# Optimization experiments

Hardware: AMD Instinct MI355X
Metric: run time of the kernel (lower is better)

## Reference

```python
import jax, jax.numpy as jnp
import numpy as np

NEG_SLOPE = 0.2  # PyG GATConv default negative_slope


def _glorot(key, shape):
    fan = shape[0]
    return jax.random.normal(key, shape, dtype=jnp.float32) / np.sqrt(fan)


def setup_inputs() -> dict:
    key = jax.random.key(0)
    ks = jax.random.split(key, 32)
    N, E, C_IN, C_H, C_OUT = 20000, 320000, 128, 640, 2
    inp = {
        "x": jax.random.normal(ks[0], (N, C_IN), dtype=jnp.float32),
        "edge_index": jax.random.randint(ks[1], (2, E), 0, N, dtype=jnp.int64),
    }
    dims = [(C_IN, C_H), (C_H, C_H), (C_H, C_H), (C_H, C_H), (C_H, C_OUT)]
    for i, (ci, co) in enumerate(dims, start=1):
        k = jax.random.split(ks[1 + i], 4)
        inp[f"W{i}"] = _glorot(k[0], (ci, co))
        inp[f"as{i}"] = _glorot(k[1], (co,))
        inp[f"ad{i}"] = _glorot(k[2], (co,))
        inp[f"b{i}"] = jnp.zeros((co,), dtype=jnp.float32)
    return inp


def _gat_conv(h, W, a_src, a_dst, b, src, dst, N):
    # h: [N, Ci] -> hW: [N, Co]
    hW = h @ W
    # per-edge attention logit: LeakyReLU(alpha_src[j] + alpha_dst[i]) for edge j->i
    e = jax.nn.leaky_relu((hW @ a_src)[src] + (hW @ a_dst)[dst], NEG_SLOPE)
    # segment softmax over incoming edges of each dst node (self-loops guarantee nonempty)
    m = jax.ops.segment_max(e, dst, num_segments=N)
    ex = jnp.exp(e - m[dst])
    den = jax.ops.segment_sum(ex, dst, num_segments=N)
    alpha = ex / den[dst]
    # weighted scatter-add of source messages
    out = jax.ops.segment_sum(alpha[:, None] * hW[src], dst, num_segments=N)
    return out + b


def reference(x, edge_index, W1, as1, ad1, b1, W2, as2, ad2, b2, W3, as3, ad3, b3,
              W4, as4, ad4, b4, W5, as5, ad5, b5):
    N = x.shape[0]
    # PyG GATConv default add_self_loops=True
    loops = jnp.arange(N, dtype=edge_index.dtype)
    ei = jnp.concatenate([edge_index, jnp.stack([loops, loops])], axis=1)
    src, dst = ei[0], ei[1]
    h = jax.nn.relu(_gat_conv(x, W1, as1, ad1, b1, src, dst, N))
    h = jax.nn.relu(_gat_conv(h, W2, as2, ad2, b2, src, dst, N))
    h = jax.nn.relu(_gat_conv(h, W3, as3, ad3, b3, src, dst, N))
    h = jax.nn.relu(_gat_conv(h, W4, as4, ad4, b4, src, dst, N))
    # dropout in eval mode = identity
    return _gat_conv(h, W5, as5, ad5, b5, src, dst, N)
```

## Files before the change

kernel.cpp:

```cpp
#include <hip/hip_runtime.h>
#include <math.h>

#define N_NODES 20000
#define MPAD 20096
#define E_EDGES 320000
#define ET (E_EDGES + N_NODES)
#define C_HID 640
#define C_IN 128
#define NEG_SLOPE 0.2f

typedef __attribute__((ext_vector_type(8))) short bf16x8;
typedef __attribute__((ext_vector_type(4))) float f32x4;

__device__ __forceinline__ float leaky(float x) { return x > 0.f ? x : NEG_SLOPE * x; }

__device__ __forceinline__ unsigned short f2bf(float f) {
    unsigned u = __float_as_uint(f);
    unsigned r = (u + 0x7fffu + ((u >> 16) & 1u)) >> 16;
    return (unsigned short)r;
}
__device__ __forceinline__ float bf2f(unsigned short h) {
    return __uint_as_float(((unsigned)h) << 16);
}

__device__ __forceinline__ void gld16(const void* g, void* l) {
    __builtin_amdgcn_global_load_lds((const __attribute__((address_space(1))) unsigned int*)g,
                                     (__attribute__((address_space(3))) unsigned int*)l,
                                     16, 0, 0);
}

__global__ void k_zero(int* p, int n) {
    int i = blockIdx.x * blockDim.x + threadIdx.x;
    if (i < n) p[i] = 0;
}

__global__ void k_zerof(float* p, int n) {
    int i = blockIdx.x * blockDim.x + threadIdx.x;
    if (i < n) p[i] = 0.f;
}

__global__ void k_count(const int* __restrict__ ei, int* __restrict__ counts) {
    int j = blockIdx.x * blockDim.x + threadIdx.x;
    if (j >= ET) return;
    int d = (j < E_EDGES) ? ei[E_EDGES + j] : (j - E_EDGES);
    atomicAdd(&counts[d], 1);
}

__global__ __launch_bounds__(1024) void k_scan(int* __restrict__ counts,
                                               int* __restrict__ rowptr) {
    __shared__ int part[1024];
    int t = threadIdx.x;
    int base = t * 20;
    int incl[20];
    int s = 0;
#pragma unroll
    for (int k = 0; k < 20; k++) {
        int i = base + k;
        int v = (i < N_NODES) ? counts[i] : 0;
        s += v;
        incl[k] = s;
    }
    part[t] = s;
    __syncthreads();
    for (int off = 1; off < 1024; off <<= 1) {
        int x = (t >= off) ? part[t - off] : 0;
        __syncthreads();
        part[t] += x;
        __syncthreads();
    }
    int prefix = (t == 0) ? 0 : part[t - 1];
    if (t == 0) rowptr[0] = 0;
#pragma unroll
    for (int k = 0; k < 20; k++) {
        int i = base + k;
        if (i < N_NODES) {
            rowptr[i + 1] = prefix + incl[k];
            counts[i] = (k == 0) ? prefix : prefix + incl[k - 1];
        }
    }
}

__global__ void k_fill(const int* __restrict__ ei, int* __restrict__ cursor, int* __restrict__ col) {
    int j = blockIdx.x * blockDim.x + threadIdx.x;
    if (j >= ET) return;
    int s, d;
    if (j < E_EDGES) { s = ei[j]; d = ei[E_EDGES + j]; }
    else { s = d = j - E_EDGES; }
    int pos = atomicAdd(&cursor[d], 1);
    col[pos] = s;
}

__global__ void k_splitW(const float* __restrict__ W, unsigned short* __restrict__ Wth,
                         unsigned short* __restrict__ Wtl, int K) {
    int idx = blockIdx.x * blockDim.x + threadIdx.x;
    if (idx >= K * C_HID) return;
    int k = idx / C_HID, n = idx - k * C_HID;
    float w = W[idx];
    unsigned short h = f2bf(w);
    Wth[n * K + k] = h;
    Wtl[n * K + k] = f2bf(w - bf2f(h));
}

__global__ void k_padzero(unsigned short* __restrict__ xah, unsigned short* __restrict__ xal,
                          unsigned short* __restrict__ ph, unsigned short* __restrict__ pl) {
    int idx = blockIdx.x * blockDim.x + threadIdx.x;
    const int nx = (MPAD - N_NODES) * C_IN;
    const int np = (MPAD - N_NODES) * C_HID;
    if (idx < nx) {
        xah[N_NODES * C_IN + idx] = 0;
        xal[N_NODES * C_IN + idx] = 0;
    }
    if (idx < np) {
        ph[N_NODES * C_HID + idx] = 0;
        pl[N_NODES * C_HID + idx] = 0;
    }
}

__global__ void k_wa(const float* __restrict__ W, const float* __restrict__ a_s,
                     const float* __restrict__ a_d,
                     float* __restrict__ ws_, float* __restrict__ wd_) {
    int wave = (blockIdx.x * blockDim.x + threadIdx.x) >> 6;
    int lane = threadIdx.x & 63;
    if (wave >= C_IN) return;
    const float* row = W + (size_t)wave * C_HID;
    float s = 0.f, d = 0.f;
#pragma unroll
    for (int c = lane; c < C_HID; c += 64) {
        float w = row[c];
        s = fmaf(w, a_s[c], s);
        d = fmaf(w, a_d[c], d);
    }
    for (int o = 32; o; o >>= 1) { s += __shfl_xor(s, o); d += __shfl_xor(d, o); }
    if (lane == 0) { ws_[wave] = s; wd_[wave] = d; }
}

__global__ __launch_bounds__(256) void k_logitx(const float* __restrict__ x,
                                                const float* __restrict__ ws_,
                                                const float* __restrict__ wd_,
                                                float* __restrict__ as_, float* __restrict__ ad_) {
    int wave = (blockIdx.x * blockDim.x + threadIdx.x) >> 6;
    int lane = threadIdx.x & 63;
    if (wave >= N_NODES) return;
    float2 xv = ((const float2*)(x + (size_t)wave * C_IN))[lane];
    float2 wsv = ((const float2*)ws_)[lane];
    float2 wdv = ((const float2*)wd_)[lane];
    float s = xv.x * wsv.x + xv.y * wsv.y;
    float d = xv.x * wdv.x + xv.y * wdv.y;
    for (int o = 32; o; o >>= 1) { s += __shfl_xor(s, o); d += __shfl_xor(d, o); }
    if (lane == 0) { as_[wave] = s; ad_[wave] = d; }
}

__global__ __launch_bounds__(256) void k_mfma_gemm(
    const unsigned short* __restrict__ Ahi, const unsigned short* __restrict__ Alo,
    const unsigned short* __restrict__ Bth, const unsigned short* __restrict__ Btl,
    float* __restrict__ C, int K, int M,
    const float* __restrict__ asrc, const float* __restrict__ adst,
    float* __restrict__ as_, float* __restrict__ ad_) {
    __shared__ unsigned short lds[4 * 128 * 32];
    const int t = threadIdx.x;
    const int lane = t & 63, wv = t >> 6;
    const int wm = wv & 1, wn = wv >> 1;
    const int quad = lane >> 4, cl = lane & 15;
    const int rowBase = blockIdx.x * 128;
    const int colBase = blockIdx.y * 128;
    const int r = t >> 2, c8 = (t & 3) * 8;

    f32x4 acc[4][4];
#pragma unroll
    for (int i = 0; i < 4; i++)
#pragma unroll
        for (int j = 0; j < 4; j++)
            acc[i][j] = (f32x4){0.f, 0.f, 0.f, 0.f};

    for (int k0 = 0; k0 < K; k0 += 32) {
        __syncthreads();
#pragma unroll
        for (int p = 0; p < 2; ++p) {
            int row = p * 64 + r;
            size_t ga = (size_t)(rowBase + row) * K + k0 + c8;
            size_t gb = (size_t)(colBase + row) * K + k0 + c8;
            int lo = row * 32 + c8;
            gld16(Ahi + ga, &lds[lo]);
            gld16(Alo + ga, &lds[4096 + lo]);
            gld16(Bth + gb, &lds[8192 + lo]);
            gld16(Btl + gb, &lds[12288 + lo]);
        }
        __syncthreads();

        bf16x8 ah[4], al[4], bh[4], bl[4];
#pragma unroll
        for (int i = 0; i < 4; ++i) {
            int am = (wm * 64 + i * 16 + cl) * 32 + quad * 8;
            ah[i] = *(const bf16x8*)&lds[am];
            al[i] = *(const bf16x8*)&lds[4096 + am];
            int bn = (wn * 64 + i * 16 + cl) * 32 + quad * 8;
            bh[i] = *(const bf16x8*)&lds[8192 + bn];
            bl[i] = *(const bf16x8*)&lds[12288 + bn];
        }
#pragma unroll
        for (int i = 0; i < 4; ++i)
#pragma unroll
            for (int j = 0; j < 4; ++j) {
                acc[i][j] = __builtin_amdgcn_mfma_f32_16x16x32_bf16(ah[i], bh[j], acc[i][j], 0, 0, 0);
                acc[i][j] = __builtin_amdgcn_mfma_f32_16x16x32_bf16(ah[i], bl[j], acc[i][j], 0, 0, 0);
                acc[i][j] = __builtin_amdgcn_mfma_f32_16x16x32_bf16(al[i], bh[j], acc[i][j], 0, 0, 0);
            }
    }

#pragma unroll
    for (int i = 0; i < 4; ++i)
#pragma unroll
        for (int j = 0; j < 4; ++j) {
            int colC = colBase + wn * 64 + j * 16 + cl;
#pragma unroll
            for (int rr = 0; rr < 4; ++rr) {
                int rowC = rowBase + wm * 64 + i * 16 + quad * 4 + rr;
                if (rowC < M) C[(size_t)rowC * C_HID + colC] = acc[i][j][rr];
            }
        }

    float av[4], dv[4];
#pragma unroll
    for (int j = 0; j < 4; ++j) {
        int cn = colBase + wn * 64 + j * 16 + cl;
        av[j] = asrc[cn];
        dv[j] = adst[cn];
    }
#pragma unroll
    for (int i = 0; i < 4; ++i)
#pragma unroll
        for (int rr = 0; rr < 4; ++rr) {
            float s = 0.f, d = 0.f;
#pragma unroll
            for (int j = 0; j < 4; ++j) {
                float v = acc[i][j][rr];
                s = fmaf(v, av[j], s);
                d = fmaf(v, dv[j], d);
            }
#pragma unroll
            for (int o = 8; o >= 1; o >>= 1) {
                s += __shfl_xor(s, o);
                d += __shfl_xor(d, o);
            }
            int rowC = rowBase + wm * 64 + i * 16 + quad * 4 + rr;
            if (cl == 0 && rowC < M) {
                atomicAdd(&as_[rowC], s);
                atomicAdd(&ad_[rowC], d);
            }
        }
}

__global__ __launch_bounds__(256) void k_mfma_gemm_pair(
    const unsigned short* __restrict__ Ahi, const unsigned short* __restrict__ Alo,
    const unsigned short* __restrict__ Bth, const unsigned short* __restrict__ Btl,
    unsigned short* __restrict__ Oh, unsigned short* __restrict__ Ol,
    const float* __restrict__ bias, int K, int M) {
    __shared__ unsigned short lds[4 * 128 * 32];
    const int t = threadIdx.x;
    const int lane = t & 63, wv = t >> 6;
    const int wm = wv & 1, wn = wv >> 1;
    const int quad = lane >> 4, cl = lane & 15;
    const int rowBase = blockIdx.x * 128;
    const int colBase = blockIdx.y * 128;
    const int r = t >> 2, c8 = (t & 3) * 8;

    f32x4 acc[4][4];
#pragma unroll
    for (int i = 0; i < 4; i++)
#pragma unroll
        for (int j = 0; j < 4; j++)
            acc[i][j] = (f32x4){0.f, 0.f, 0.f, 0.f};

    for (int k0 = 0; k0 < K; k0 += 32) {
        __syncthreads();
#pragma unroll
        for (int p = 0; p < 2; ++p) {
            int row = p * 64 + r;
            size_t ga = (size_t)(rowBase + row) * K + k0 + c8;
            size_t gb = (size_t)(colBase + row) * K + k0 + c8;
            int lo = row * 32 + c8;
            gld16(Ahi + ga, &lds[lo]);
            gld16(Alo + ga, &lds[4096 + lo]);
            gld16(Bth + gb, &lds[8192 + lo]);
            gld16(Btl + gb, &lds[12288 + lo]);
        }
        __syncthreads();

        bf16x8 ah[4], al[4], bh[4], bl[4];
#pragma unroll
        for (int i = 0; i < 4; ++i) {
            int am = (wm * 64 + i * 16 + cl) * 32 + quad * 8;
            ah[i] = *(const bf16x8*)&lds[am];
            al[i] = *(const bf16x8*)&lds[4096 + am];
            int bn = (wn * 64 + i * 16 + cl) * 32 + quad * 8;
            bh[i] = *(const bf16x8*)&lds[8192 + bn];
            bl[i] = *(const bf16x8*)&lds[12288 + bn];
        }
#pragma unroll
        for (int i = 0; i < 4; ++i)
#pragma unroll
            for (int j = 0; j < 4; ++j) {
                acc[i][j] = __builtin_amdgcn_mfma_f32_16x16x32_bf16(ah[i], bh[j], acc[i][j], 0, 0, 0);
                acc[i][j] = __builtin_amdgcn_mfma_f32_16x16x32_bf16(ah[i], bl[j], acc[i][j], 0, 0, 0);
                acc[i][j] = __builtin_amdgcn_mfma_f32_16x16x32_bf16(al[i], bh[j], acc[i][j], 0, 0, 0);
            }
    }

#pragma unroll
    for (int j = 0; j < 4; ++j) {
        int colC = colBase + wn * 64 + j * 16 + cl;
        float bv = bias[colC];
#pragma unroll
        for (int i = 0; i < 4; ++i)
#pragma unroll
            for (int rr = 0; rr < 4; ++rr) {
                int rowC = rowBase + wm * 64 + i * 16 + quad * 4 + rr;
                if (rowC < M) {
                    float v = fmaxf(acc[i][j][rr] + bv, 0.f);
                    unsigned short h = f2bf(v);
                    Oh[(size_t)rowC * C_HID + colC] = h;
                    Ol[(size_t)rowC * C_HID + colC] = f2bf(v - bf2f(h));
                }
            }
    }
}

__global__ __launch_bounds__(256) void k_gather(const float* __restrict__ hW,
                                                const float* __restrict__ as_,
                                                const float* __restrict__ ad_,
                                                const int* __restrict__ rowptr,
                                                const int* __restrict__ col,
                                                const float* __restrict__ bias,
                                                unsigned short* __restrict__ outh,
                                                unsigned short* __restrict__ outl) {
    int wv = threadIdx.x >> 6, lane = threadIdx.x & 63;
    int node = blockIdx.x * 4 + wv;
    int c = blockIdx.y;
    if (node >= N_NODES) return;
    int start = rowptr[node], end = rowptr[node + 1];
    int deg = end - start;
    const float* base = hW + c * 128 + lane * 2;
    float ax = 0.f, ay = 0.f;
    float adi = ad_[node];

    if (deg <= 64) {
        int col_v = col[start + min(lane, deg - 1)];
        float asv = as_[col_v];
        float logit = (lane < deg) ? leaky(asv + adi) : -1e30f;
        float m = logit;
#pragma unroll
        for (int o = 32; o; o >>= 1) m = fmaxf(m, __shfl_xor(m, o));
        float ex = __expf(logit - m);
        float den = ex;
#pragma unroll
        for (int o = 32; o; o >>= 1) den += __shfl_xor(den, o);
        float alpha_v = ex / den;

        for (int e0 = 0; e0 < deg; e0 += 8) {
            float2 r[8];
            float a[8];
#pragma unroll
            for (int q = 0; q < 8; ++q) {
                int e = e0 + q;
                int ec = min(e, deg - 1);
                int s = __shfl(col_v, ec);
                float ar = __shfl(alpha_v, ec);
                a[q] = (e < deg) ? ar : 0.f;
                r[q] = *(const float2*)(base + (size_t)s * C_HID);
            }
#pragma unroll
            for (int q = 0; q < 8; ++q) {
                ax = fmaf(a[q], r[q].x, ax);
                ay = fmaf(a[q], r[q].y, ay);
            }
        }
    } else {
        float m = -1e30f;
        for (int j = start + lane; j < end; j += 64)
            m = fmaxf(m, leaky(as_[col[j]] + adi));
        for (int o = 32; o; o >>= 1) m = fmaxf(m, __shfl_xor(m, o));
        float den = 0.f;
        for (int j = start + lane; j < end; j += 64)
            den += __expf(leaky(as_[col[j]] + adi) - m);
        for (int o = 32; o; o >>= 1) den += __shfl_xor(den, o);
        float inv = 1.f / den;
        for (int j = start; j < end; ++j) {
            int s = col[j];
            float a = __expf(leaky(as_[s] + adi) - m) * inv;
            float2 r = *(const float2*)(base + (size_t)s * C_HID);
            ax = fmaf(a, r.x, ax);
            ay = fmaf(a, r.y, ay);
        }
    }

    float2 b = *(const float2*)&bias[c * 128 + lane * 2];
    float v0 = fmaxf(ax + b.x, 0.f);
    float v1 = fmaxf(ay + b.y, 0.f);
    unsigned short h0 = f2bf(v0), h1 = f2bf(v1);
    size_t o = (size_t)node * C_HID + c * 128 + lane * 2;
    *(ushort2*)&outh[o] = make_ushort2(h0, h1);
    *(ushort2*)&outl[o] = make_ushort2(f2bf(v0 - bf2f(h0)), f2bf(v1 - bf2f(h1)));
}

__global__ __launch_bounds__(256) void k_gather_x(const float* __restrict__ x,
                                                  const float* __restrict__ as_,
                                                  const float* __restrict__ ad_,
                                                  const int* __restrict__ rowptr,
                                                  const int* __restrict__ col,
                                                  unsigned short* __restrict__ outh,
                                                  unsigned short* __restrict__ outl) {
    int wv = threadIdx.x >> 6, lane = threadIdx.x & 63;
    int node = blockIdx.x * 4 + wv;
    if (node >= N_NODES) return;
    int start = rowptr[node], end = rowptr[node + 1];
    int deg = end - start;
    const float* base = x + lane * 2;
    float ax = 0.f, ay = 0.f;
    float adi = ad_[node];

    if (deg <= 64) {
        int col_v = col[start + min(lane, deg - 1)];
        float asv = as_[col_v];
        float logit = (lane < deg) ? leaky(asv + adi) : -1e30f;
        float m = logit;
#pragma unroll
        for (int o = 32; o; o >>= 1) m = fmaxf(m, __shfl_xor(m, o));
        float ex = __expf(logit - m);
        float den = ex;
#pragma unroll
        for (int o = 32; o; o >>= 1) den += __shfl_xor(den, o);
        float alpha_v = ex / den;

        for (int e0 = 0; e0 < deg; e0 += 8) {
            float2 r[8];
            float a[8];
#pragma unroll
            for (int q = 0; q < 8; ++q) {
                int e = e0 + q;
                int ec = min(e, deg - 1);
                int s = __shfl(col_v, ec);
                float ar = __shfl(alpha_v, ec);
                a[q] = (e < deg) ? ar : 0.f;
                r[q] = *(const float2*)(base + (size_t)s * C_IN);
            }
#pragma unroll
            for (int q = 0; q < 8; ++q) {
                ax = fmaf(a[q], r[q].x, ax);
                ay = fmaf(a[q], r[q].y, ay);
            }
        }
    } else {
        float m = -1e30f;
        for (int j = start + lane; j < end; j += 64)
            m = fmaxf(m, leaky(as_[col[j]] + adi));
        for (int o = 32; o; o >>= 1) m = fmaxf(m, __shfl_xor(m, o));
        float den = 0.f;
        for (int j = start + lane; j < end; j += 64)
            den += __expf(leaky(as_[col[j]] + adi) - m);
        for (int o = 32; o; o >>= 1) den += __shfl_xor(den, o);
        float inv = 1.f / den;
        for (int j = start; j < end; ++j) {
            int s = col[j];
            float a = __expf(leaky(as_[s] + adi) - m) * inv;
            float2 r = *(const float2*)(base + (size_t)s * C_IN);
            ax = fmaf(a, r.x, ax);
            ay = fmaf(a, r.y, ay);
        }
    }

    unsigned short h0 = f2bf(ax), h1 = f2bf(ay);
    size_t o = (size_t)node * C_IN + lane * 2;
    *(ushort2*)&outh[o] = make_ushort2(h0, h1);
    *(ushort2*)&outl[o] = make_ushort2(f2bf(ax - bf2f(h0)), f2bf(ay - bf2f(h1)));
}

__global__ __launch_bounds__(256) void k_gemm2(const unsigned short* __restrict__ hh,
                                               const unsigned short* __restrict__ hl,
                                               const float* __restrict__ W,
                                               const float* __restrict__ asrc,
                                               const float* __restrict__ adst,
                                               float* __restrict__ hW5,
                                               float* __restrict__ as_,
                                               float* __restrict__ ad_) {
    int wave = (blockIdx.x * blockDim.x + threadIdx.x) >> 6;
    int lane = threadIdx.x & 63;
    if (wave >= N_NODES) return;
    const ushort2* rh = (const ushort2*)(hh + (size_t)wave * C_HID);
    const ushort2* rl = (const ushort2*)(hl + (size_t)wave * C_HID);
    float a0 = 0.f, a1 = 0.f;
#pragma unroll
    for (int k2 = lane; k2 < C_HID / 2; k2 += 64) {
        ushort2 h2 = rh[k2];
        ushort2 l2 = rl[k2];
        float v0 = bf2f(h2.x) + bf2f(l2.x);
        float v1 = bf2f(h2.y) + bf2f(l2.y);
        int k = k2 * 2;
        a0 = fmaf(v0, W[k * 2 + 0], a0);
        a1 = fmaf(v0, W[k * 2 + 1], a1);
        a0 = fmaf(v1, W[k * 2 + 2], a0);
        a1 = fmaf(v1, W[k * 2 + 3], a1);
    }
    for (int o = 32; o; o >>= 1) { a0 += __shfl_xor(a0, o); a1 += __shfl_xor(a1, o); }
    if (lane == 0) {
        hW5[wave * 2 + 0] = a0;
        hW5[wave * 2 + 1] = a1;
        as_[wave] = a0 * asrc[0] + a1 * asrc[1];
        ad_[wave] = a0 * adst[0] + a1 * adst[1];
    }
}

__global__ __launch_bounds__(256) void k_agg2(const float* __restrict__ hW5,
                                              const float* __restrict__ as_,
                                              const float* __restrict__ ad_,
                                              const int* __restrict__ rowptr,
                                              const int* __restrict__ col,
                                              const float* __restrict__ bias,
                                              float* __restrict__ out) {
    int wv = threadIdx.x >> 6, lane = threadIdx.x & 63;
    int node = blockIdx.x * 4 + wv;
    if (node >= N_NODES) return;
    int start = rowptr[node], end = rowptr[node + 1];
    int deg = end - start;
    float adi = ad_[node];
    float o0, o1;
    if (deg <= 64) {
        int cv = col[start + min(lane, deg - 1)];
        float logit = (lane < deg) ? leaky(as_[cv] + adi) : -1e30f;
        float m = logit;
#pragma unroll
        for (int o = 32; o; o >>= 1) m = fmaxf(m, __shfl_xor(m, o));
        float ex = __expf(logit - m);
        float den = ex;
#pragma unroll
        for (int o = 32; o; o >>= 1) den += __shfl_xor(den, o);
        float al = ex / den;
        float2 hv = make_float2(0.f, 0.f);
        if (lane < deg) hv = *(const float2*)&hW5[cv * 2];
        o0 = al * hv.x; o1 = al * hv.y;
#pragma unroll
        for (int o = 32; o; o >>= 1) { o0 += __shfl_xor(o0, o); o1 += __shfl_xor(o1, o); }
    } else {
        float m = -1e30f;
        for (int j = start + lane; j < end; j += 64)
            m = fmaxf(m, leaky(as_[col[j]] + adi));
        for (int o = 32; o; o >>= 1) m = fmaxf(m, __shfl_xor(m, o));
        float den = 0.f;
        for (int j = start + lane; j < end; j += 64)
            den += __expf(leaky(as_[col[j]] + adi) - m);
        for (int o = 32; o; o >>= 1) den += __shfl_xor(den, o);
        float inv = 1.f / den;
        o0 = 0.f; o1 = 0.f;
        for (int j = start + lane; j < end; j += 64) {
            int s = col[j];
            float al = __expf(leaky(as_[s] + adi) - m) * inv;
            o0 = fmaf(al, hW5[s * 2 + 0], o0);
            o1 = fmaf(al, hW5[s * 2 + 1], o1);
        }
        for (int o = 32; o; o >>= 1) { o0 += __shfl_xor(o0, o); o1 += __shfl_xor(o1, o); }
    }
    if (lane == 0) {
        out[node * 2 + 0] = o0 + bias[0];
        out[node * 2 + 1] = o1 + bias[1];
    }
}

extern "C" void kernel_launch(void* const* d_in, const int* in_sizes, int n_in,
                              void* d_out, int out_size, void* d_ws, size_t ws_size,
                              hipStream_t stream) {
    const float* x   = (const float*)d_in[0];
    const int*   ei  = (const int*)d_in[1];
    const float* W[5]  = {(const float*)d_in[2],  (const float*)d_in[6],
                          (const float*)d_in[10], (const float*)d_in[14],
                          (const float*)d_in[18]};
    const float* As[5] = {(const float*)d_in[3],  (const float*)d_in[7],
                          (const float*)d_in[11], (const float*)d_in[15],
                          (const float*)d_in[19]};
    const float* Ad[5] = {(const float*)d_in[4],  (const float*)d_in[8],
                          (const float*)d_in[12], (const float*)d_in[16],
                          (const float*)d_in[20]};
    const float* Bi[5] = {(const float*)d_in[5],  (const float*)d_in[9],
                          (const float*)d_in[13], (const float*)d_in[17],
                          (const float*)d_in[21]};
    float* out = (float*)d_out;

    char* w = (char*)d_ws;
    float* bufX = (float*)w;                 w += (size_t)N_NODES * C_HID * 4;
    unsigned short* xa_hi = (unsigned short*)bufX;
    unsigned short* xa_lo = xa_hi + (size_t)MPAD * C_IN;
    unsigned short* pair_hi = (unsigned short*)w; w += (size_t)MPAD * C_HID * 2;
    unsigned short* pair_lo = (unsigned short*)w; w += (size_t)MPAD * C_HID * 2;
    unsigned short* Wth = (unsigned short*)w;     w += (size_t)C_HID * C_HID * 2;
    unsigned short* Wtl = (unsigned short*)w;     w += (size_t)C_HID * C_HID * 2;
    float* as_  = (float*)w;  w += N_NODES * 4;
    float* ad_  = (float*)w;  w += N_NODES * 4;
    float* hW5  = (float*)w;  w += N_NODES * 2 * 4;
    float* ws_  = (float*)w;  w += C_IN * 4;
    float* wd_  = (float*)w;  w += C_IN * 4;
    int* rowptr = (int*)w;    w += (N_NODES + 1) * 4 + 12;
    int* counts = (int*)w;    w += N_NODES * 4;
    int* col    = (int*)w;    w += ET * 4;

    const int TB = 256;
    k_zero<<<(N_NODES + TB - 1) / TB, TB, 0, stream>>>(counts, N_NODES);
    k_count<<<(ET + TB - 1) / TB, TB, 0, stream>>>(ei, counts);
    k_scan<<<1, 1024, 0, stream>>>(counts, rowptr);
    k_fill<<<(ET + TB - 1) / TB, TB, 0, stream>>>(ei, counts, col);

    k_padzero<<<((MPAD - N_NODES) * C_HID + TB - 1) / TB, TB, 0, stream>>>(xa_hi, xa_lo, pair_hi, pair_lo);

    dim3 gemmGrid(MPAD / 128, C_HID / 128);
    dim3 gathGrid(N_NODES / 4, 5);
    int nodeWaveBlocks = (N_NODES + 3) / 4;

    k_splitW<<<(C_IN * C_HID + TB - 1) / TB, TB, 0, stream>>>(W[0], Wth, Wtl, C_IN);
    k_wa<<<32, TB, 0, stream>>>(W[0], As[0], Ad[0], ws_, wd_);
    k_logitx<<<nodeWaveBlocks, TB, 0, stream>>>(x, ws_, wd_, as_, ad_);
    k_gather_x<<<nodeWaveBlocks, TB, 0, stream>>>(x, as_, ad_, rowptr, col, xa_hi, xa_lo);
    k_mfma_gemm_pair<<<gemmGrid, TB, 0, stream>>>(xa_hi, xa_lo, Wth, Wtl,
                                                  pair_hi, pair_lo, Bi[0], C_IN, N_NODES);

    for (int l = 1; l <= 3; ++l) {
        k_zerof<<<(2 * N_NODES + TB - 1) / TB, TB, 0, stream>>>(as_, 2 * N_NODES);
        k_splitW<<<(C_HID * C_HID + TB - 1) / TB, TB, 0, stream>>>(W[l], Wth, Wtl, C_HID);
        k_mfma_gemm<<<gemmGrid, TB, 0, stream>>>(pair_hi, pair_lo, Wth, Wtl, bufX, C_HID, N_NODES,
                                                 As[l], Ad[l], as_, ad_);
        k_gather<<<gathGrid, TB, 0, stream>>>(bufX, as_, ad_, rowptr, col, Bi[l], pair_hi, pair_lo);
    }

    k_gemm2<<<nodeWaveBlocks, TB, 0, stream>>>(pair_hi, pair_lo, W[4], As[4], Ad[4], hW5, as_, ad_);
    k_agg2<<<nodeWaveBlocks, TB, 0, stream>>>(hW5, as_, ad_, rowptr, col, Bi[4], out);
}
```

Measured before the change: 814.9 us.

## Use 128x64 GEMM tiles with swizzled block order and tiled weight transpose

The MFMA GEMM kernels shrink from 128x128 to 128x64 output tiles, using a 1D grid with a grouped block-index decode so neighbouring blocks share A row tiles. This doubles the block count to 1570 so more CUs stay busy, at the cost of reloading A tiles twice as often. The weight split/transpose kernel is rewritten to stage through a padded shared-memory tile, giving coalesced float4 reads and vectorized ushort4 writes in place of strided scalar stores.

```diff
diff --git a/kernel.cpp b/kernel.cpp
--- a/kernel.cpp
+++ b/kernel.cpp
@@ -9,6 +9,11 @@
 #define C_IN 128
 #define NEG_SLOPE 0.2f
 
+#define NXB 157
+#define NYB 10
+#define NXB_FULL 152
+#define IDS_MAIN 1520
+
 typedef __attribute__((ext_vector_type(8))) short bf16x8;
 typedef __attribute__((ext_vector_type(4))) float f32x4;
 
@@ -27,6 +32,18 @@
     __builtin_amdgcn_global_load_lds((const __attribute__((address_space(1))) unsigned int*)g,
                                      (__attribute__((address_space(3))) unsigned int*)l,
                                      16, 0, 0);
+}
+
+__device__ __forceinline__ void decode_xy(int id, int& bx, int& by) {
+    if (id < IDS_MAIN) {
+        int g = id / 80;
+        bx = g * 8 + (id & 7);
+        by = (id % 80) >> 3;
+    } else {
+        int v = id - IDS_MAIN;
+        bx = NXB_FULL + v % 5;
+        by = v / 5;
+    }
 }
 
 __global__ void k_zero(int* p, int n) {
@@ -90,15 +107,37 @@
     col[pos] = s;
 }
 
-__global__ void k_splitW(const float* __restrict__ W, unsigned short* __restrict__ Wth,
-                         unsigned short* __restrict__ Wtl, int K) {
-    int idx = blockIdx.x * blockDim.x + threadIdx.x;
-    if (idx >= K * C_HID) return;
-    int k = idx / C_HID, n = idx - k * C_HID;
-    float w = W[idx];
-    unsigned short h = f2bf(w);
-    Wth[n * K + k] = h;
-    Wtl[n * K + k] = f2bf(w - bf2f(h));
+__global__ __launch_bounds__(256) void k_splitWT(const float* __restrict__ W,
+                                                 unsigned short* __restrict__ Wth,
+                                                 unsigned short* __restrict__ Wtl, int K) {
+    __shared__ float tile[64][65];
+    int t = threadIdx.x;
+    int ki = blockIdx.x * 64, ni = blockIdx.y * 64;
+    int tr = t >> 2;
+    int tc = (t & 3) * 16;
+#pragma unroll
+    for (int q = 0; q < 4; ++q) {
+        float4 v = *(const float4*)&W[(size_t)(ki + tr) * C_HID + ni + tc + q * 4];
+        tile[tr][tc + q * 4 + 0] = v.x;
+        tile[tr][tc + q * 4 + 1] = v.y;
+        tile[tr][tc + q * 4 + 2] = v.z;
+        tile[tr][tc + q * 4 + 3] = v.w;
+    }
+    __syncthreads();
+    unsigned short hh[16], ll[16];
+#pragma unroll
+    for (int j = 0; j < 16; ++j) {
+        float w = tile[tc + j][tr];
+        unsigned short h = f2bf(w);
+        hh[j] = h;
+        ll[j] = f2bf(w - bf2f(h));
+    }
+    size_t o = (size_t)(ni + tr) * K + ki + tc;
+#pragma unroll
+    for (int q = 0; q < 4; ++q) {
+        *(ushort4*)&Wth[o + q * 4] = make_ushort4(hh[q*4], hh[q*4+1], hh[q*4+2], hh[q*4+3]);
+        *(ushort4*)&Wtl[o + q * 4] = make_ushort4(ll[q*4], ll[q*4+1], ll[q*4+2], ll[q*4+3]);
+    }
 }
 
 __global__ void k_padzero(unsigned short* __restrict__ xah, unsigned short* __restrict__ xal,
@@ -156,51 +195,59 @@
     float* __restrict__ C, int K, int M,
     const float* __restrict__ asrc, const float* __restrict__ adst,
     float* __restrict__ as_, float* __restrict__ ad_) {
-    __shared__ unsigned short lds[4 * 128 * 32];
+    __shared__ unsigned short lds[12288];
     const int t = threadIdx.x;
     const int lane = t & 63, wv = t >> 6;
-    const int wm = wv & 1, wn = wv >> 1;
+    const int wm = wv >> 1, wn = wv & 1;
     const int quad = lane >> 4, cl = lane & 15;
-    const int rowBase = blockIdx.x * 128;
-    const int colBase = blockIdx.y * 128;
-    const int r = t >> 2, c8 = (t & 3) * 8;
-
-    f32x4 acc[4][4];
+    int bx, by;
+    decode_xy(blockIdx.x, bx, by);
+    const int rowBase = bx * 128;
+    const int colBase = by * 64;
+    const int r4 = t >> 2, c8 = (t & 3) * 8;
+
+    f32x4 acc[4][2];
 #pragma unroll
     for (int i = 0; i < 4; i++)
 #pragma unroll
-        for (int j = 0; j < 4; j++)
+        for (int j = 0; j < 2; j++)
             acc[i][j] = (f32x4){0.f, 0.f, 0.f, 0.f};
 
     for (int k0 = 0; k0 < K; k0 += 32) {
         __syncthreads();
 #pragma unroll
         for (int p = 0; p < 2; ++p) {
-            int row = p * 64 + r;
+            int row = p * 64 + r4;
             size_t ga = (size_t)(rowBase + row) * K + k0 + c8;
-            size_t gb = (size_t)(colBase + row) * K + k0 + c8;
             int lo = row * 32 + c8;
             gld16(Ahi + ga, &lds[lo]);
             gld16(Alo + ga, &lds[4096 + lo]);
+        }
+        {
+            size_t gb = (size_t)(colBase + r4) * K + k0 + c8;
+            int lo = r4 * 32 + c8;
             gld16(Bth + gb, &lds[8192 + lo]);
-            gld16(Btl + gb, &lds[12288 + lo]);
+            gld16(Btl + gb, &lds[10240 + lo]);
         }
         __syncthreads();
 
-        bf16x8 ah[4], al[4], bh[4], bl[4];
+        bf16x8 ah[4], al[4], bh[2], bl[2];
 #pragma unroll
         for (int i = 0; i < 4; ++i) {
             int am = (wm * 64 + i * 16 + cl) * 32 + quad * 8;
             ah[i] = *(const bf16x8*)&lds[am];
             al[i] = *(const bf16x8*)&lds[4096 + am];
-            int bn = (wn * 64 + i * 16 + cl) * 32 + quad * 8;
-            bh[i] = *(const bf16x8*)&lds[8192 + bn];
-            bl[i] = *(const bf16x8*)&lds[12288 + bn];
+        }
+#pragma unroll
+        for (int j = 0; j < 2; ++j) {
+            int bn = (wn * 32 + j * 16 + cl) * 32 + quad * 8;
+            bh[j] = *(const bf16x8*)&lds[8192 + bn];
+            bl[j] = *(const bf16x8*)&lds[10240 + bn];
         }
 #pragma unroll
         for (int i = 0; i < 4; ++i)
 #pragma unroll
-            for (int j = 0; j < 4; ++j) {
+            for (int j = 0; j < 2; ++j) {
                 acc[i][j] = __builtin_amdgcn_mfma_f32_16x16x32_bf16(ah[i], bh[j], acc[i][j], 0, 0, 0);
                 acc[i][j] = __builtin_amdgcn_mfma_f32_16x16x32_bf16(ah[i], bl[j], acc[i][j], 0, 0, 0);
                 acc[i][j] = __builtin_amdgcn_mfma_f32_16x16x32_bf16(al[i], bh[j], acc[i][j], 0, 0, 0);
@@ -210,8 +257,8 @@
 #pragma unroll
     for (int i = 0; i < 4; ++i)
 #pragma unroll
-        for (int j = 0; j < 4; ++j) {
-            int colC = colBase + wn * 64 + j * 16 + cl;
+        for (int j = 0; j < 2; ++j) {
+            int colC = colBase + wn * 32 + j * 16 + cl;
 #pragma unroll
             for (int rr = 0; rr < 4; ++rr) {
                 int rowC = rowBase + wm * 64 + i * 16 + quad * 4 + rr;
@@ -219,10 +266,10 @@
             }
         }
 
-    float av[4], dv[4];
-#pragma unroll
-    for (int j = 0; j < 4; ++j) {
-        int cn = colBase + wn * 64 + j * 16 + cl;
+    float av[2], dv[2];
+#pragma unroll
+    for (int j = 0; j < 2; ++j) {
+        int cn = colBase + wn * 32 + j * 16 + cl;
         av[j] = asrc[cn];
         dv[j] = adst[cn];
     }
@@ -232,7 +279,7 @@
         for (int rr = 0; rr < 4; ++rr) {
             float s = 0.f, d = 0.f;
 #pragma unroll
-            for (int j = 0; j < 4; ++j) {
+            for (int j = 0; j < 2; ++j) {
                 float v = acc[i][j][rr];
                 s = fmaf(v, av[j], s);
                 d = fmaf(v, dv[j], d);
@@ -255,51 +302,59 @@
     const unsigned short* __restrict__ Bth, const unsigned short* __restrict__ Btl,
     unsigned short* __restrict__ Oh, unsigned short* __restrict__ Ol,
     const float* __restrict__ bias, int K, int M) {
-    __shared__ unsigned short lds[4 * 128 * 32];
+    __shared__ unsigned short lds[12288];
     const int t = threadIdx.x;
     const int lane = t & 63, wv = t >> 6;
-    const int wm = wv & 1, wn = wv >> 1;
+    const int wm = wv >> 1, wn = wv & 1;
     const int quad = lane >> 4, cl = lane & 15;
-    const int rowBase = blockIdx.x * 128;
-    const int colBase = blockIdx.y * 128;
-    const int r = t >> 2, c8 = (t & 3) * 8;
-
-    f32x4 acc[4][4];
+    int bx, by;
+    decode_xy(blockIdx.x, bx, by);
+    const int rowBase = bx * 128;
+    const int colBase = by * 64;
+    const int r4 = t >> 2, c8 = (t & 3) * 8;
+
+    f32x4 acc[4][2];
 #pragma unroll
     for (int i = 0; i < 4; i++)
 #pragma unroll
-        for (int j = 0; j < 4; j++)
+        for (int j = 0; j < 2; j++)
             acc[i][j] = (f32x4){0.f, 0.f, 0.f, 0.f};
 
     for (int k0 = 0; k0 < K; k0 += 32) {
         __syncthreads();
 #pragma unroll
         for (int p = 0; p < 2; ++p) {
-            int row = p * 64 + r;
+            int row = p * 64 + r4;
             size_t ga = (size_t)(rowBase + row) * K + k0 + c8;
-            size_t gb = (size_t)(colBase + row) * K + k0 + c8;
             int lo = row * 32 + c8;
             gld16(Ahi + ga, &lds[lo]);
             gld16(Alo + ga, &lds[4096 + lo]);
+        }
+        {
+            size_t gb = (size_t)(colBase + r4) * K + k0 + c8;
+            int lo = r4 * 32 + c8;
             gld16(Bth + gb, &lds[8192 + lo]);
-            gld16(Btl + gb, &lds[12288 + lo]);
+            gld16(Btl + gb, &lds[10240 + lo]);
         }
         __syncthreads();
 
-        bf16x8 ah[4], al[4], bh[4], bl[4];
+        bf16x8 ah[4], al[4], bh[2], bl[2];
 #pragma unroll
         for (int i = 0; i < 4; ++i) {
             int am = (wm * 64 + i * 16 + cl) * 32 + quad * 8;
             ah[i] = *(const bf16x8*)&lds[am];
             al[i] = *(const bf16x8*)&lds[4096 + am];
-            int bn = (wn * 64 + i * 16 + cl) * 32 + quad * 8;
-            bh[i] = *(const bf16x8*)&lds[8192 + bn];
-            bl[i] = *(const bf16x8*)&lds[12288 + bn];
+        }
+#pragma unroll
+        for (int j = 0; j < 2; ++j) {
+            int bn = (wn * 32 + j * 16 + cl) * 32 + quad * 8;
+            bh[j] = *(const bf16x8*)&lds[8192 + bn];
+            bl[j] = *(const bf16x8*)&lds[10240 + bn];
         }
 #pragma unroll
         for (int i = 0; i < 4; ++i)
 #pragma unroll
-            for (int j = 0; j < 4; ++j) {
+            for (int j = 0; j < 2; ++j) {
                 acc[i][j] = __builtin_amdgcn_mfma_f32_16x16x32_bf16(ah[i], bh[j], acc[i][j], 0, 0, 0);
                 acc[i][j] = __builtin_amdgcn_mfma_f32_16x16x32_bf16(ah[i], bl[j], acc[i][j], 0, 0, 0);
                 acc[i][j] = __builtin_amdgcn_mfma_f32_16x16x32_bf16(al[i], bh[j], acc[i][j], 0, 0, 0);
@@ -307,8 +362,8 @@
     }
 
 #pragma unroll
-    for (int j = 0; j < 4; ++j) {
-        int colC = colBase + wn * 64 + j * 16 + cl;
+    for (int j = 0; j < 2; ++j) {
+        int colC = colBase + wn * 32 + j * 16 + cl;
         float bv = bias[colC];
 #pragma unroll
         for (int i = 0; i < 4; ++i)
@@ -608,22 +663,22 @@
 
     k_padzero<<<((MPAD - N_NODES) * C_HID + TB - 1) / TB, TB, 0, stream>>>(xa_hi, xa_lo, pair_hi, pair_lo);
 
-    dim3 gemmGrid(MPAD / 128, C_HID / 128);
+    const int gemmBlocks = NXB * NYB;
     dim3 gathGrid(N_NODES / 4, 5);
     int nodeWaveBlocks = (N_NODES + 3) / 4;
 
-    k_splitW<<<(C_IN * C_HID + TB - 1) / TB, TB, 0, stream>>>(W[0], Wth, Wtl, C_IN);
+    k_splitWT<<<dim3(C_IN / 64, C_HID / 64), TB, 0, stream>>>(W[0], Wth, Wtl, C_IN);
     k_wa<<<32, TB, 0, stream>>>(W[0], As[0], Ad[0], ws_, wd_);
     k_logitx<<<nodeWaveBlocks, TB, 0, stream>>>(x, ws_, wd_, as_, ad_);
     k_gather_x<<<nodeWaveBlocks, TB, 0, stream>>>(x, as_, ad_, rowptr, col, xa_hi, xa_lo);
-    k_mfma_gemm_pair<<<gemmGrid, TB, 0, stream>>>(xa_hi, xa_lo, Wth, Wtl,
-                                                  pair_hi, pair_lo, Bi[0], C_IN, N_NODES);
+    k_mfma_gemm_pair<<<gemmBlocks, TB, 0, stream>>>(xa_hi, xa_lo, Wth, Wtl,
+                                                    pair_hi, pair_lo, Bi[0], C_IN, N_NODES);
 
     for (int l = 1; l <= 3; ++l) {
         k_zerof<<<(2 * N_NODES + TB - 1) / TB, TB, 0, stream>>>(as_, 2 * N_NODES);
-        k_splitW<<<(C_HID * C_HID + TB - 1) / TB, TB, 0, stream>>>(W[l], Wth, Wtl, C_HID);
-        k_mfma_gemm<<<gemmGrid, TB, 0, stream>>>(pair_hi, pair_lo, Wth, Wtl, bufX, C_HID, N_NODES,
-                                                 As[l], Ad[l], as_, ad_);
+        k_splitWT<<<dim3(C_HID / 64, C_HID / 64), TB, 0, stream>>>(W[l], Wth, Wtl, C_HID);
+        k_mfma_gemm<<<gemmBlocks, TB, 0, stream>>>(pair_hi, pair_lo, Wth, Wtl, bufX, C_HID, N_NODES,
+                                                   As[l], Ad[l], as_, ad_);
         k_gather<<<gathGrid, TB, 0, stream>>>(bufX, as_, ad_, rowptr, col, Bi[l], pair_hi, pair_lo);
     }
 
```

After: 764.7 us. -6.2%, faster.
